# Optimization experiments

Measured on AMD Instinct MI355X. Metric: run time of the kernel, lower is better.

Reference implementation:

```python
import jax, jax.numpy as jnp
import numpy as np

B, S, DIM, H, HD = 2, 2048, 512, 8, 64
VD = DIM // H  # 64
QK = H * HD


def setup_inputs() -> dict:
    key = jax.random.key(0)
    k1, k2, k3, k4, k5 = jax.random.split(key, 5)
    x = jax.random.normal(k1, (B, S, DIM), dtype=jnp.float32)
    mask = jax.random.bernoulli(k2, 0.5, (B, S))
    # per-position rotation matrices, scaled to keep activations O(1)
    rotator = jax.random.normal(k3, (B, S, HD, HD), dtype=jnp.float32) / np.sqrt(HD)
    # torch Linear weights: [out_features, in_features], no bias
    W_trans = jax.random.normal(k4, (2 * QK + DIM, DIM), dtype=jnp.float32) / np.sqrt(DIM)
    W_o = jax.random.normal(k5, (DIM, DIM), dtype=jnp.float32) / np.sqrt(DIM)
    return {"x": x, "mask": mask, "rotator": rotator, "W_trans": W_trans, "W_o": W_o}


def _taylor_attention(qs, ks, vs, mask):
    # 2nd-order Taylor approximation of exp for softmax weights
    # qs/ks: [B,S,H,HD], vs: [B,S,H,VD], mask: [B,S] key mask
    scores = jnp.einsum('bqhd,bkhd->bhqk', qs, ks) / np.sqrt(HD)
    w = 1.0 + scores + 0.5 * scores * scores
    w = jnp.where(mask[:, None, None, :], w, 0.0)
    w = w / jnp.sum(w, axis=-1, keepdims=True)
    out = jnp.einsum('bhqk,bkhd->bqhd', w, vs)
    return out.reshape(out.shape[0], out.shape[1], -1)  # [B,S,DIM]


def reference(x, mask, rotator, W_trans, W_o):
    t = x @ W_trans.T  # [B,S,2*QK+DIM]
    qs = t[..., :QK].reshape(B, S, H, HD)
    ks = t[..., QK:2 * QK].reshape(B, S, H, HD)
    vs = t[..., 2 * QK:].reshape(B, S, H, VD)
    sel = mask[..., None, None]
    qs = jnp.where(sel, jnp.einsum('bsij,bshj->bshi', rotator, qs), qs)
    ks = jnp.where(sel, jnp.einsum('bsij,bshj->bshi', rotator, ks), ks)
    out = _taylor_attention(qs, ks, vs, mask)
    return out @ W_o.T
```

## Files before the change

kernel.cpp:

```cpp
#include <hip/hip_runtime.h>
#include <hip/hip_bf16.h>

#define B_    2
#define S_    2048
#define DIM_  512
#define H_    8
#define HD_   64
#define TOUT_ 1536
#define ROWS_ (B_ * S_)

typedef unsigned short ushort_t;
typedef __attribute__((ext_vector_type(8))) __bf16 bf16x8;
typedef __attribute__((ext_vector_type(4))) float floatx4;

#define AS_GLB __attribute__((address_space(1)))
#define AS_LDS __attribute__((address_space(3)))

__device__ __forceinline__ unsigned short f2bfu(float f) {
    unsigned u = __float_as_uint(f);
    unsigned r = (u + 0x7fffu + ((u >> 16) & 1u)) >> 16;
    return (unsigned short)r;
}
__device__ __forceinline__ bf16x8 cvt8(const float* p) {
    float4 a = *reinterpret_cast<const float4*>(p);
    float4 b = *reinterpret_cast<const float4*>(p + 4);
    ushort_t o[8] = {f2bfu(a.x), f2bfu(a.y), f2bfu(a.z), f2bfu(a.w),
                     f2bfu(b.x), f2bfu(b.y), f2bfu(b.z), f2bfu(b.w)};
    return *reinterpret_cast<bf16x8*>(o);
}

__global__ void tmha_mask(const unsigned char* mb, int* wm) {
    __shared__ int s_bf, s_f, s_u8;
    int tid = threadIdx.x;
    if (tid == 0) { s_bf = 0; s_f = 0; s_u8 = 0; }
    __syncthreads();
    int cbf = 0, cf = 0, cu8 = 0;
    for (int i = tid; i < 4096; i += 256) {
        unsigned char v = mb[i];
        if (v == 0x3F || v == 0x80) {
            cf++;
            if ((i & 3) == 1) cbf++;
        } else if (v != 0 && (i & 3) != 0) {
            cu8++;
        }
    }
    atomicAdd(&s_bf, cbf); atomicAdd(&s_f, cf); atomicAdd(&s_u8, cu8);
    __syncthreads();
    int cls = (s_bf > 0) ? 2 : (s_f > 0) ? 3 : (s_u8 > 0) ? 0 : 1;
    for (int i = tid; i < ROWS_; i += 256) {
        int v;
        if (cls == 0)      v = (mb[i] != 0);
        else if (cls == 1) v = (reinterpret_cast<const int*>(mb)[i] != 0);
        else if (cls == 2) v = ((reinterpret_cast<const unsigned short*>(mb)[i] & 0x7fffu) != 0);
        else               v = ((reinterpret_cast<const unsigned int*>(mb)[i] & 0x7fffffffu) != 0);
        wm[i] = v;
    }
}

#define XN4_  (ROWS_ * DIM_ / 4)
#define WTN4_ (TOUT_ * DIM_ / 4)
#define WON4_ (DIM_ * DIM_ / 4)
__global__ __launch_bounds__(256) void cast3_bf16(const float* __restrict__ x,
                                                  const float* __restrict__ wt,
                                                  const float* __restrict__ wo,
                                                  ushort_t* __restrict__ xb,
                                                  ushort_t* __restrict__ wtb,
                                                  ushort_t* __restrict__ wob) {
    int i = blockIdx.x * 256 + threadIdx.x;
    const float* s; ushort_t* d; int off;
    if (i < XN4_)              { s = x;  d = xb;  off = i; }
    else if (i < XN4_ + WTN4_) { s = wt; d = wtb; off = i - XN4_; }
    else                       { s = wo; d = wob; off = i - XN4_ - WTN4_; }
    float4 v = reinterpret_cast<const float4*>(s)[off];
    ushort_t o[4] = {f2bfu(v.x), f2bfu(v.y), f2bfu(v.z), f2bfu(v.w)};
    reinterpret_cast<uint2*>(d)[off] = *reinterpret_cast<uint2*>(o);
}

template <int TM, int N, int K, bool OUT_BF16>
__global__ __launch_bounds__(256) void mfma_gemm_bt(const ushort_t* __restrict__ A,
                                                    const ushort_t* __restrict__ Bm,
                                                    void* __restrict__ Cout) {
    constexpr int FM = (TM + 31) / 32;
    __shared__ __align__(16) ushort_t As[TM * 64];
    __shared__ __align__(16) ushort_t Bs[128 * 64];
    int tid = threadIdx.x;
    int lane = tid & 63;
    int wv = tid >> 6;
    int wm = wv >> 1, wn = wv & 1;
    int quad = lane >> 4;
    int mrow = lane & 15;
    int bx = blockIdx.x;
    int by = blockIdx.y;

    floatx4 acc[FM][4];
#pragma unroll
    for (int i = 0; i < FM; i++)
#pragma unroll
        for (int j = 0; j < 4; j++) acc[i][j] = (floatx4){0.f, 0.f, 0.f, 0.f};

    for (int k0 = 0; k0 < K; k0 += 64) {
#pragma unroll
        for (int t = 0; t < TM / 32; t++) {
            int p = (wv * (TM / 32) + t) * 64 + lane;
            int row = p >> 3, cp = p & 7;
            int gc = cp ^ (row & 7);
            const ushort_t* ga = A + (size_t)(by * TM + row) * K + k0 + gc * 8;
            __builtin_amdgcn_global_load_lds((const AS_GLB unsigned int*)ga,
                                             (AS_LDS unsigned int*)&As[(size_t)(wv * (TM / 32) + t) * 64 * 8],
                                             16, 0, 0);
        }
#pragma unroll
        for (int t = 0; t < 4; t++) {
            int p = (wv * 4 + t) * 64 + lane;
            int row = p >> 3, cp = p & 7;
            int gc = cp ^ (row & 7);
            const ushort_t* gb = Bm + (size_t)(bx * 128 + row) * K + k0 + gc * 8;
            __builtin_amdgcn_global_load_lds((const AS_GLB unsigned int*)gb,
                                             (AS_LDS unsigned int*)&Bs[(size_t)(wv * 4 + t) * 64 * 8],
                                             16, 0, 0);
        }
        __syncthreads();
#pragma unroll
        for (int ks = 0; ks < 64; ks += 32) {
            int c = (ks >> 3) + quad;
            bf16x8 af[FM], bf[4];
#pragma unroll
            for (int i = 0; i < FM; i++) {
                int row = wm * (TM / 2) + i * 16 + mrow;
                int pos = row * 8 + (c ^ (row & 7));
                af[i] = *reinterpret_cast<const bf16x8*>(&As[pos * 8]);
            }
#pragma unroll
            for (int j = 0; j < 4; j++) {
                int row = wn * 64 + j * 16 + mrow;
                int pos = row * 8 + (c ^ (row & 7));
                bf[j] = *reinterpret_cast<const bf16x8*>(&Bs[pos * 8]);
            }
#pragma unroll
            for (int i = 0; i < FM; i++)
#pragma unroll
                for (int j = 0; j < 4; j++)
                    acc[i][j] = __builtin_amdgcn_mfma_f32_16x16x32_bf16(af[i], bf[j], acc[i][j], 0, 0, 0);
        }
        __syncthreads();
    }

    int col0 = bx * 128 + wn * 64 + mrow;
    int row0 = by * TM + wm * (TM / 2) + quad * 4;
    if constexpr (OUT_BF16) {
        ushort_t* C = reinterpret_cast<ushort_t*>(Cout);
#pragma unroll
        for (int i = 0; i < FM; i++)
#pragma unroll
            for (int j = 0; j < 4; j++)
#pragma unroll
                for (int r = 0; r < 4; r++)
                    C[(size_t)(row0 + i * 16 + r) * N + col0 + j * 16] = f2bfu(acc[i][j][r]);
    } else {
        float* C = reinterpret_cast<float*>(Cout);
#pragma unroll
        for (int i = 0; i < FM; i++)
#pragma unroll
            for (int j = 0; j < 4; j++)
#pragma unroll
                for (int r = 0; r < 4; r++)
                    C[(size_t)(row0 + i * 16 + r) * N + col0 + j * 16] = acc[i][j][r];
    }
}

__global__ __launch_bounds__(256) void rot_qk_mfma(const ushort_t* __restrict__ t,
                                                   const float* __restrict__ rotG,
                                                   const int* __restrict__ wm,
                                                   ushort_t* __restrict__ Qb,
                                                   ushort_t* __restrict__ Kb) {
    int lane = threadIdx.x & 63;
    int wv = threadIdx.x >> 6;
    int row = blockIdx.x * 4 + wv;
    int b = row >> 11, s = row & 2047;
    int lm = lane & 15, quad = lane >> 4;
    const ushort_t* trow = t + (size_t)row * TOUT_;
    int kb = s >> 4, l = s & 15;

    if (wm[row]) {
        bf16x8 af[2];
#pragma unroll
        for (int kc = 0; kc < 2; kc++)
            af[kc] = *reinterpret_cast<const bf16x8*>(trow + lm * 64 + kc * 32 + quad * 8);

        const float* R = rotG + (size_t)row * 4096;
        floatx4 dacc[4];
#pragma unroll
        for (int nb = 0; nb < 4; nb++) dacc[nb] = (floatx4){0.f, 0.f, 0.f, 0.f};
#pragma unroll
        for (int nb = 0; nb < 4; nb++)
#pragma unroll
            for (int kc = 0; kc < 2; kc++) {
                bf16x8 bfr = cvt8(R + (size_t)(nb * 16 + lm) * 64 + kc * 32 + quad * 8);
                dacc[nb] = __builtin_amdgcn_mfma_f32_16x16x32_bf16(af[kc], bfr, dacc[nb], 0, 0, 0);
            }
#pragma unroll
        for (int nb = 0; nb < 4; nb++)
#pragma unroll
            for (int r = 0; r < 4; r++) {
                int vec = quad * 4 + r;
                int hh = vec & 7;
                ushort_t v = f2bfu(dacc[nb][r]);
                if (vec >= 8) {
                    int c = nb * 2 + (lm >> 3), e = lm & 7;
                    Kb[(((size_t)(b * 8 + hh) * 128 + kb) * 8 + c) * 128 + l * 8 + e] = v;
                } else {
                    Qb[((size_t)(b * 8 + hh) * 2048 + s) * 64 + nb * 16 + lm] = v;
                }
            }
    } else {
#pragma unroll
        for (int nb = 0; nb < 4; nb++)
#pragma unroll
            for (int r = 0; r < 4; r++) {
                int vec = quad * 4 + r;
                int hh = vec & 7;
                ushort_t v = trow[vec * 64 + nb * 16 + lm];
                if (vec >= 8) {
                    int c = nb * 2 + (lm >> 3), e = lm & 7;
                    Kb[(((size_t)(b * 8 + hh) * 128 + kb) * 8 + c) * 128 + l * 8 + e] = v;
                } else {
                    Qb[((size_t)(b * 8 + hh) * 2048 + s) * 64 + nb * 16 + lm] = v;
                }
            }
    }
}

__global__ __launch_bounds__(256) void prep_vt(const ushort_t* __restrict__ t,
                                               const int* __restrict__ wm,
                                               ushort_t* __restrict__ VtG) {
    __shared__ ushort_t tile[64][72];
    __shared__ float mrow[64];
    int st = blockIdx.x;
    int bh = blockIdx.y;
    int b = bh >> 3, h = bh & 7;
    int tid = threadIdx.x;
    if (tid < 64) mrow[tid] = wm[b * 2048 + st * 64 + tid] ? 1.0f : 0.0f;
#pragma unroll
    for (int i = 0; i < 2; i++) {
        int q = i * 256 + tid;
        int r = q >> 3, c8 = (q & 7) * 8;
        uint4 v = *reinterpret_cast<const uint4*>(
            t + (size_t)(b * 2048 + st * 64 + r) * TOUT_ + 1024 + h * 64 + c8);
        *reinterpret_cast<uint4*>(&tile[r][c8]) = v;
    }
    __syncthreads();
#pragma unroll
    for (int i = 0; i < 8; i++) {
        int e = i * 256 + tid;
        int d = e >> 5, sl = (e & 31) * 2;
        unsigned u0 = (mrow[sl]     != 0.f) ? (unsigned)tile[sl][d]     : 0u;
        unsigned u1 = (mrow[sl + 1] != 0.f) ? (unsigned)tile[sl + 1][d] : 0u;
        *reinterpret_cast<unsigned int*>(VtG + ((size_t)bh * 65 + d) * 2048 + st * 64 + sl) = u0 | (u1 << 16);
    }
    if (tid < 32) {
        int sl = tid * 2;
        unsigned m0 = mrow[sl]     != 0.f ? 0x3F80u : 0u;
        unsigned m1 = mrow[sl + 1] != 0.f ? 0x3F80u : 0u;
        *reinterpret_cast<unsigned int*>(VtG + ((size_t)bh * 65 + 64) * 2048 + st * 64 + sl) = m0 | (m1 << 16);
    }
}

__global__ __launch_bounds__(256) void tmha_attn_mfma(const ushort_t* __restrict__ Qb,
                                                      const ushort_t* __restrict__ KbF,
                                                      const ushort_t* __restrict__ VtG,
                                                      float* __restrict__ numer,
                                                      float* __restrict__ den) {
    __shared__ __align__(16) ushort_t Vs[2][520 * 8];
    __shared__ __align__(16) ushort_t Ps[512 * 8];
    int tid = threadIdx.x;
    int lane = tid & 63;
    int wv = tid >> 6;
    int lm = lane & 15;
    int quad = lane >> 4;
    int qt = blockIdx.x;
    int h = blockIdx.y;
    int z = blockIdx.z;
    int b = z >> 1;
    int ks = z & 1;
    int bh = b * 8 + h;

    const ushort_t* Kf  = KbF + (size_t)bh * 128 * 1024;
    const ushort_t* Vbh = VtG + (size_t)bh * 65 * 2048;

    bf16x8 qf[2];
    {
        const ushort_t* qp = Qb + ((size_t)bh * 2048 + qt * 64 + wv * 16 + lm) * 64 + quad * 8;
        qf[0] = *reinterpret_cast<const bf16x8*>(qp);
        qf[1] = *reinterpret_cast<const bf16x8*>(qp + 32);
    }

    bf16x8 vzero;
    *reinterpret_cast<uint4*>(&vzero) = (uint4){0u, 0u, 0u, 0u};

    floatx4 oacc[5];
#pragma unroll
    for (int j = 0; j < 5; j++) oacc[j] = (floatx4){0.f, 0.f, 0.f, 0.f};

    bf16x8 kr[4][2];
    auto loadK = [&](int kt) {
        int kb = kt >> 4;
#pragma unroll
        for (int j = 0; j < 4; j++)
#pragma unroll
            for (int kc = 0; kc < 2; kc++)
                kr[j][kc] = *reinterpret_cast<const bf16x8*>(
                    Kf + (((size_t)(kb + j) * 8 + kc * 4 + quad) * 16 + lm) * 8);
    };
    auto stageV = [&](int buf, int kt) {
#pragma unroll
        for (int t4 = 0; t4 < 2; t4++) {
            int p = (wv * 2 + t4) * 64 + lane;
            int row = p >> 3, cp = p & 7;
            int gc = cp ^ (row & 7);
            const ushort_t* g = Vbh + (size_t)row * 2048 + kt + gc * 8;
            __builtin_amdgcn_global_load_lds((const AS_GLB unsigned int*)g,
                                             (AS_LDS unsigned int*)&Vs[buf][(wv * 2 + t4) * 64 * 8],
                                             16, 0, 0);
        }
        if (tid < 8) {
            const ushort_t* g = Vbh + (size_t)64 * 2048 + kt + tid * 8;
            __builtin_amdgcn_global_load_lds((const AS_GLB unsigned int*)g,
                                             (AS_LDS unsigned int*)&Vs[buf][512 * 8],
                                             16, 0, 0);
        }
    };

    int kt0 = ks * 1024;
    stageV(0, kt0);
    loadK(kt0);
    int buf = 0;
#pragma unroll 1
    for (int tt = 0; tt < 16; tt++) {
        int ktn = (tt == 15) ? kt0 : kt0 + (tt + 1) * 64;
        __syncthreads();
        stageV(buf ^ 1, ktn);

        floatx4 sacc[4];
#pragma unroll
        for (int j = 0; j < 4; j++) sacc[j] = (floatx4){0.f, 0.f, 0.f, 0.f};
#pragma unroll
        for (int j = 0; j < 4; j++)
#pragma unroll
            for (int kc = 0; kc < 2; kc++)
                sacc[j] = __builtin_amdgcn_mfma_f32_16x16x32_bf16(qf[kc], kr[j][kc], sacc[j], 0, 0, 0);

        loadK(ktn);

#pragma unroll
        for (int j = 0; j < 4; j++)
#pragma unroll
            for (int r = 0; r < 4; r++) {
                float s = sacc[j][r];
                float wgt = fmaf(s, fmaf(s, 0.0078125f, 0.125f), 1.0f);
                int m = wv * 16 + quad * 4 + r;
                int col = j * 16 + lm;
                int cw = col >> 3;
                int pos = m * 8 + (cw ^ (m & 7));
                Ps[pos * 8 + (col & 7)] = f2bfu(wgt);
            }
        asm volatile("s_waitcnt lgkmcnt(0)" ::: "memory");
        __builtin_amdgcn_sched_barrier(0);

        int qrow_l = wv * 16 + lm;
        bf16x8 pa[2];
#pragma unroll
        for (int kc = 0; kc < 2; kc++) {
            int c = kc * 4 + quad;
            int ppos = qrow_l * 8 + (c ^ (qrow_l & 7));
            pa[kc] = *reinterpret_cast<const bf16x8*>(&Ps[ppos * 8]);
        }
#pragma unroll
        for (int j = 0; j < 5; j++) {
            int vrow = (j < 4) ? (j * 16 + lm) : 64;
#pragma unroll
            for (int kc = 0; kc < 2; kc++) {
                int c = kc * 4 + quad;
                int vpos = vrow * 8 + (c ^ (vrow & 7));
                bf16x8 vb = *reinterpret_cast<const bf16x8*>(&Vs[buf][vpos * 8]);
                if (j == 4 && lm != 0) vb = vzero;
                oacc[j] = __builtin_amdgcn_mfma_f32_16x16x32_bf16(pa[kc], vb, oacc[j], 0, 0, 0);
            }
        }
        buf ^= 1;
    }

#pragma unroll
    for (int j = 0; j < 4; j++)
#pragma unroll
        for (int r = 0; r < 4; r++) {
            int qrow = b * 2048 + qt * 64 + wv * 16 + quad * 4 + r;
            numer[((size_t)ks * ROWS_ + qrow) * DIM_ + h * 64 + j * 16 + lm] = oacc[j][r];
        }
    if (lm == 0) {
#pragma unroll
        for (int r = 0; r < 4; r++) {
            int qrow = b * 2048 + qt * 64 + wv * 16 + quad * 4 + r;
            den[((size_t)ks * ROWS_ + qrow) * 8 + h] = oacc[4][r];
        }
    }
}

__global__ __launch_bounds__(256) void attn_combine(const float* __restrict__ numer,
                                                    const float* __restrict__ den,
                                                    ushort_t* __restrict__ attnAb) {
    int i = blockIdx.x * 256 + threadIdx.x;
    int row = i >> 7;
    int c4 = (i & 127) * 4;
    int h = c4 >> 6;
    float4 n0 = *reinterpret_cast<const float4*>(&numer[(size_t)row * DIM_ + c4]);
    float4 n1 = *reinterpret_cast<const float4*>(&numer[((size_t)ROWS_ + row) * DIM_ + c4]);
    float d = den[(size_t)row * 8 + h] + den[((size_t)ROWS_ + row) * 8 + h];
    float inv = 1.0f / d;
    ushort_t o[4] = {f2bfu((n0.x + n1.x) * inv), f2bfu((n0.y + n1.y) * inv),
                     f2bfu((n0.z + n1.z) * inv), f2bfu((n0.w + n1.w) * inv)};
    *reinterpret_cast<uint2*>(&attnAb[(size_t)row * DIM_ + c4]) = *reinterpret_cast<uint2*>(o);
}

extern "C" void kernel_launch(void* const* d_in, const int* in_sizes, int n_in,
                              void* d_out, int out_size, void* d_ws, size_t ws_size,
                              hipStream_t stream) {
    (void)in_sizes; (void)n_in; (void)out_size; (void)ws_size;
    const float* x    = (const float*)d_in[0];
    const void*  mask = d_in[1];
    const float* rot  = (const float*)d_in[2];
    const float* Wt   = (const float*)d_in[3];
    const float* Wo   = (const float*)d_in[4];

    char* ws = (char*)d_ws;
    int* wmask       = (int*)(ws + 64);
    ushort_t* t      = (ushort_t*)(ws + 32768);
    ushort_t* Xb     = (ushort_t*)(ws + 25198592);
    ushort_t* Wtb    = (ushort_t*)(ws + 29392896);
    ushort_t* Wob    = (ushort_t*)(ws + 30965760);
    ushort_t* Qb     = (ushort_t*)(ws + 31490048);
    ushort_t* Kb     = (ushort_t*)(ws + 35684352);
    ushort_t* VtG    = (ushort_t*)(ws + 39878656);
    ushort_t* attnAb = (ushort_t*)(ws + 44138496);
    float* numer     = (float*)(ws + 32768);
    float* den       = (float*)(ws + 32768 + 16777216);

    tmha_mask<<<1, 256, 0, stream>>>((const unsigned char*)mask, wmask);

    cast3_bf16<<<(XN4_ + WTN4_ + WON4_) / 256, 256, 0, stream>>>(x, Wt, Wo, Xb, Wtb, Wob);

    {
        dim3 grid(TOUT_ / 128, ROWS_ / 64);
        mfma_gemm_bt<64, TOUT_, DIM_, true><<<grid, 256, 0, stream>>>(Xb, Wtb, (void*)t);
    }

    rot_qk_mfma<<<ROWS_ / 4, 256, 0, stream>>>(t, rot, wmask, Qb, Kb);

    {
        dim3 grid(32, 16);
        prep_vt<<<grid, 256, 0, stream>>>(t, wmask, VtG);
    }

    {
        dim3 grid(32, 8, 4);
        tmha_attn_mfma<<<grid, 256, 0, stream>>>(Qb, Kb, VtG, numer, den);
    }
    attn_combine<<<(ROWS_ * 128) / 256, 256, 0, stream>>>(numer, den, attnAb);

    {
        dim3 grid(DIM_ / 128, ROWS_ / 32);
        mfma_gemm_bt<32, DIM_, DIM_, false><<<grid, 256, 0, stream>>>(attnAb, Wob, d_out);
    }
}
```

Before: 194.0 us.

## Fuse mask into cast kernel, fold combine into output GEMM, retune attention pipeline

The mask-decoding kernel is folded into the input cast kernel as an extra block, so one launch is saved. The split-K combine (summing the two partial numerators and denominators, then normalizing) moves into the A-tile load of the output GEMM, which removes a kernel and the bf16 round trip of the intermediate. The attention loop becomes a manually unrolled ping-pong with separate V buffers. It reads the mask row straight from global memory instead of LDS, adds setprio around the MFMAs and uses an explicit vmcnt wait plus barrier. The cost is that the output GEMM now does the fp32 reads and the reduction redundantly for each of its 4 column blocks.

```diff
diff --git a/kernel.cpp b/kernel.cpp
--- a/kernel.cpp
+++ b/kernel.cpp
@@ -29,43 +29,46 @@
     return *reinterpret_cast<bf16x8*>(o);
 }
 
-__global__ void tmha_mask(const unsigned char* mb, int* wm) {
-    __shared__ int s_bf, s_f, s_u8;
-    int tid = threadIdx.x;
-    if (tid == 0) { s_bf = 0; s_f = 0; s_u8 = 0; }
-    __syncthreads();
-    int cbf = 0, cf = 0, cu8 = 0;
-    for (int i = tid; i < 4096; i += 256) {
-        unsigned char v = mb[i];
-        if (v == 0x3F || v == 0x80) {
-            cf++;
-            if ((i & 3) == 1) cbf++;
-        } else if (v != 0 && (i & 3) != 0) {
-            cu8++;
-        }
-    }
-    atomicAdd(&s_bf, cbf); atomicAdd(&s_f, cf); atomicAdd(&s_u8, cu8);
-    __syncthreads();
-    int cls = (s_bf > 0) ? 2 : (s_f > 0) ? 3 : (s_u8 > 0) ? 0 : 1;
-    for (int i = tid; i < ROWS_; i += 256) {
-        int v;
-        if (cls == 0)      v = (mb[i] != 0);
-        else if (cls == 1) v = (reinterpret_cast<const int*>(mb)[i] != 0);
-        else if (cls == 2) v = ((reinterpret_cast<const unsigned short*>(mb)[i] & 0x7fffu) != 0);
-        else               v = ((reinterpret_cast<const unsigned int*>(mb)[i] & 0x7fffffffu) != 0);
-        wm[i] = v;
-    }
-}
-
 #define XN4_  (ROWS_ * DIM_ / 4)
 #define WTN4_ (TOUT_ * DIM_ / 4)
 #define WON4_ (DIM_ * DIM_ / 4)
-__global__ __launch_bounds__(256) void cast3_bf16(const float* __restrict__ x,
-                                                  const float* __restrict__ wt,
-                                                  const float* __restrict__ wo,
-                                                  ushort_t* __restrict__ xb,
-                                                  ushort_t* __restrict__ wtb,
-                                                  ushort_t* __restrict__ wob) {
+#define CASTBLKS_ ((XN4_ + WTN4_ + WON4_) / 256)
+__global__ __launch_bounds__(256) void prep_inputs(const float* __restrict__ x,
+                                                   const float* __restrict__ wt,
+                                                   const float* __restrict__ wo,
+                                                   const unsigned char* __restrict__ mb,
+                                                   ushort_t* __restrict__ xb,
+                                                   ushort_t* __restrict__ wtb,
+                                                   ushort_t* __restrict__ wob,
+                                                   int* __restrict__ wm) {
+    if (blockIdx.x >= CASTBLKS_) {
+        __shared__ int s_bf, s_f, s_u8;
+        int tid = threadIdx.x;
+        if (tid == 0) { s_bf = 0; s_f = 0; s_u8 = 0; }
+        __syncthreads();
+        int cbf = 0, cf = 0, cu8 = 0;
+        for (int i = tid; i < 4096; i += 256) {
+            unsigned char v = mb[i];
+            if (v == 0x3F || v == 0x80) {
+                cf++;
+                if ((i & 3) == 1) cbf++;
+            } else if (v != 0 && (i & 3) != 0) {
+                cu8++;
+            }
+        }
+        atomicAdd(&s_bf, cbf); atomicAdd(&s_f, cf); atomicAdd(&s_u8, cu8);
+        __syncthreads();
+        int cls = (s_bf > 0) ? 2 : (s_f > 0) ? 3 : (s_u8 > 0) ? 0 : 1;
+        for (int i = tid; i < ROWS_; i += 256) {
+            int v;
+            if (cls == 0)      v = (mb[i] != 0);
+            else if (cls == 1) v = (reinterpret_cast<const int*>(mb)[i] != 0);
+            else if (cls == 2) v = ((reinterpret_cast<const unsigned short*>(mb)[i] & 0x7fffu) != 0);
+            else               v = ((reinterpret_cast<const unsigned int*>(mb)[i] & 0x7fffffffu) != 0);
+            wm[i] = v;
+        }
+        return;
+    }
     int i = blockIdx.x * 256 + threadIdx.x;
     const float* s; ushort_t* d; int off;
     if (i < XN4_)              { s = x;  d = xb;  off = i; }
@@ -168,6 +171,90 @@
     }
 }
 
+__global__ __launch_bounds__(256) void gemm2_fused(const float* __restrict__ numer,
+                                                   const float* __restrict__ den,
+                                                   const ushort_t* __restrict__ Bm,
+                                                   float* __restrict__ C) {
+    constexpr int TM = 32, N = DIM_, K = DIM_;
+    __shared__ __align__(16) ushort_t As[TM * 64];
+    __shared__ __align__(16) ushort_t Bs[128 * 64];
+    int tid = threadIdx.x;
+    int lane = tid & 63;
+    int wv = tid >> 6;
+    int wm = wv >> 1, wn = wv & 1;
+    int quad = lane >> 4;
+    int mrow = lane & 15;
+    int bx = blockIdx.x;
+    int by = blockIdx.y;
+
+    floatx4 acc[4];
+#pragma unroll
+    for (int j = 0; j < 4; j++) acc[j] = (floatx4){0.f, 0.f, 0.f, 0.f};
+
+    for (int k0 = 0; k0 < K; k0 += 64) {
+        {
+            int p = tid;
+            int row = p >> 3, cp = p & 7;
+            int arow = by * TM + row;
+            int col0 = k0 + cp * 8;
+            int hh = col0 >> 6;
+            float dsum = den[(size_t)arow * 8 + hh] + den[((size_t)ROWS_ + arow) * 8 + hh];
+            float inv = 1.0f / dsum;
+            const float* n0 = &numer[(size_t)arow * DIM_ + col0];
+            const float* n1 = &numer[((size_t)ROWS_ + arow) * DIM_ + col0];
+            float4 a0 = *reinterpret_cast<const float4*>(n0);
+            float4 a1 = *reinterpret_cast<const float4*>(n0 + 4);
+            float4 b0 = *reinterpret_cast<const float4*>(n1);
+            float4 b1 = *reinterpret_cast<const float4*>(n1 + 4);
+            ushort_t o[8] = {f2bfu((a0.x + b0.x) * inv), f2bfu((a0.y + b0.y) * inv),
+                             f2bfu((a0.z + b0.z) * inv), f2bfu((a0.w + b0.w) * inv),
+                             f2bfu((a1.x + b1.x) * inv), f2bfu((a1.y + b1.y) * inv),
+                             f2bfu((a1.z + b1.z) * inv), f2bfu((a1.w + b1.w) * inv)};
+            int pos = row * 8 + (cp ^ (row & 7));
+            *reinterpret_cast<uint4*>(&As[pos * 8]) = *reinterpret_cast<const uint4*>(o);
+        }
+#pragma unroll
+        for (int t = 0; t < 4; t++) {
+            int p = (wv * 4 + t) * 64 + lane;
+            int row = p >> 3, cp = p & 7;
+            int gc = cp ^ (row & 7);
+            const ushort_t* gb = Bm + (size_t)(bx * 128 + row) * K + k0 + gc * 8;
+            __builtin_amdgcn_global_load_lds((const AS_GLB unsigned int*)gb,
+                                             (AS_LDS unsigned int*)&Bs[(size_t)(wv * 4 + t) * 64 * 8],
+                                             16, 0, 0);
+        }
+        __syncthreads();
+#pragma unroll
+        for (int ks = 0; ks < 64; ks += 32) {
+            int c = (ks >> 3) + quad;
+            bf16x8 af, bf[4];
+            {
+                int row = wm * 16 + mrow;
+                int pos = row * 8 + (c ^ (row & 7));
+                af = *reinterpret_cast<const bf16x8*>(&As[pos * 8]);
+            }
+#pragma unroll
+            for (int j = 0; j < 4; j++) {
+                int row = wn * 64 + j * 16 + mrow;
+                int pos = row * 8 + (c ^ (row & 7));
+                bf[j] = *reinterpret_cast<const bf16x8*>(&Bs[pos * 8]);
+            }
+#pragma unroll
+            for (int j = 0; j < 4; j++)
+                acc[j] = __builtin_amdgcn_mfma_f32_16x16x32_bf16(af, bf[j], acc[j], 0, 0, 0);
+        }
+        __syncthreads();
+    }
+
+    int col0 = bx * 128 + wn * 64 + mrow;
+    int row0 = by * TM + wm * 16 + quad * 4;
+#pragma unroll
+    for (int j = 0; j < 4; j++)
+#pragma unroll
+        for (int r = 0; r < 4; r++)
+            C[(size_t)(row0 + r) * N + col0 + j * 16] = acc[j][r];
+}
+
 __global__ __launch_bounds__(256) void rot_qk_mfma(const ushort_t* __restrict__ t,
                                                    const float* __restrict__ rotG,
                                                    const int* __restrict__ wm,
@@ -270,7 +357,8 @@
                                                       const ushort_t* __restrict__ VtG,
                                                       float* __restrict__ numer,
                                                       float* __restrict__ den) {
-    __shared__ __align__(16) ushort_t Vs[2][520 * 8];
+    __shared__ __align__(16) ushort_t VsA[512 * 8];
+    __shared__ __align__(16) ushort_t VsB[512 * 8];
     __shared__ __align__(16) ushort_t Ps[512 * 8];
     int tid = threadIdx.x;
     int lane = tid & 63;
@@ -284,8 +372,9 @@
     int ks = z & 1;
     int bh = b * 8 + h;
 
-    const ushort_t* Kf  = KbF + (size_t)bh * 128 * 1024;
-    const ushort_t* Vbh = VtG + (size_t)bh * 65 * 2048;
+    const ushort_t* Kf   = KbF + (size_t)bh * 128 * 1024;
+    const ushort_t* Vbh  = VtG + (size_t)bh * 65 * 2048;
+    const ushort_t* Mrow = Vbh + (size_t)64 * 2048;
 
     bf16x8 qf[2];
     {
@@ -311,7 +400,7 @@
                 kr[j][kc] = *reinterpret_cast<const bf16x8*>(
                     Kf + (((size_t)(kb + j) * 8 + kc * 4 + quad) * 16 + lm) * 8);
     };
-    auto stageV = [&](int buf, int kt) {
+    auto stageV = [&](ushort_t* Vw, int kt) {
 #pragma unroll
         for (int t4 = 0; t4 < 2; t4++) {
             int p = (wv * 2 + t4) * 64 + lane;
@@ -319,35 +408,30 @@
             int gc = cp ^ (row & 7);
             const ushort_t* g = Vbh + (size_t)row * 2048 + kt + gc * 8;
             __builtin_amdgcn_global_load_lds((const AS_GLB unsigned int*)g,
-                                             (AS_LDS unsigned int*)&Vs[buf][(wv * 2 + t4) * 64 * 8],
+                                             (AS_LDS unsigned int*)&Vw[(wv * 2 + t4) * 64 * 8],
                                              16, 0, 0);
         }
-        if (tid < 8) {
-            const ushort_t* g = Vbh + (size_t)64 * 2048 + kt + tid * 8;
-            __builtin_amdgcn_global_load_lds((const AS_GLB unsigned int*)g,
-                                             (AS_LDS unsigned int*)&Vs[buf][512 * 8],
-                                             16, 0, 0);
-        }
     };
 
-    int kt0 = ks * 1024;
-    stageV(0, kt0);
-    loadK(kt0);
-    int buf = 0;
-#pragma unroll 1
-    for (int tt = 0; tt < 16; tt++) {
-        int ktn = (tt == 15) ? kt0 : kt0 + (tt + 1) * 64;
-        __syncthreads();
-        stageV(buf ^ 1, ktn);
+    auto tile = [&](const ushort_t* Vr, ushort_t* Vw, int kt, int ktn) {
+        bf16x8 mvb[2];
+#pragma unroll
+        for (int kc = 0; kc < 2; kc++)
+            mvb[kc] = *reinterpret_cast<const bf16x8*>(Mrow + kt + (kc * 4 + quad) * 8);
+        __builtin_amdgcn_sched_barrier(0);
+        stageV(Vw, ktn);
+        __builtin_amdgcn_sched_barrier(0);
 
         floatx4 sacc[4];
 #pragma unroll
         for (int j = 0; j < 4; j++) sacc[j] = (floatx4){0.f, 0.f, 0.f, 0.f};
+        __builtin_amdgcn_s_setprio(1);
 #pragma unroll
         for (int j = 0; j < 4; j++)
 #pragma unroll
             for (int kc = 0; kc < 2; kc++)
                 sacc[j] = __builtin_amdgcn_mfma_f32_16x16x32_bf16(qf[kc], kr[j][kc], sacc[j], 0, 0, 0);
+        __builtin_amdgcn_s_setprio(0);
 
         loadK(ktn);
 
@@ -374,19 +458,41 @@
             int ppos = qrow_l * 8 + (c ^ (qrow_l & 7));
             pa[kc] = *reinterpret_cast<const bf16x8*>(&Ps[ppos * 8]);
         }
-#pragma unroll
-        for (int j = 0; j < 5; j++) {
-            int vrow = (j < 4) ? (j * 16 + lm) : 64;
+        __builtin_amdgcn_s_setprio(1);
+#pragma unroll
+        for (int j = 0; j < 4; j++) {
+            int vrow = j * 16 + lm;
 #pragma unroll
             for (int kc = 0; kc < 2; kc++) {
                 int c = kc * 4 + quad;
                 int vpos = vrow * 8 + (c ^ (vrow & 7));
-                bf16x8 vb = *reinterpret_cast<const bf16x8*>(&Vs[buf][vpos * 8]);
-                if (j == 4 && lm != 0) vb = vzero;
+                bf16x8 vb = *reinterpret_cast<const bf16x8*>(&Vr[vpos * 8]);
                 oacc[j] = __builtin_amdgcn_mfma_f32_16x16x32_bf16(pa[kc], vb, oacc[j], 0, 0, 0);
             }
         }
-        buf ^= 1;
+#pragma unroll
+        for (int kc = 0; kc < 2; kc++) {
+            bf16x8 vb = (lm == 0) ? mvb[kc] : vzero;
+            oacc[4] = __builtin_amdgcn_mfma_f32_16x16x32_bf16(pa[kc], vb, oacc[4], 0, 0, 0);
+        }
+        __builtin_amdgcn_s_setprio(0);
+
+        __builtin_amdgcn_sched_barrier(0);
+        asm volatile("s_waitcnt vmcnt(8)" ::: "memory");
+        __builtin_amdgcn_s_barrier();
+    };
+
+    int kt0 = ks * 1024;
+    stageV(VsA, kt0);
+    loadK(kt0);
+    __syncthreads();
+#pragma unroll 1
+    for (int tt = 0; tt < 8; tt++) {
+        int kt = kt0 + tt * 128;
+        int kt1 = kt + 64;
+        int kt2 = (tt == 7) ? kt0 : kt + 128;
+        tile(VsA, VsB, kt, kt1);
+        tile(VsB, VsA, kt1, kt2);
     }
 
 #pragma unroll
@@ -403,22 +509,6 @@
             den[((size_t)ks * ROWS_ + qrow) * 8 + h] = oacc[4][r];
         }
     }
-}
-
-__global__ __launch_bounds__(256) void attn_combine(const float* __restrict__ numer,
-                                                    const float* __restrict__ den,
-                                                    ushort_t* __restrict__ attnAb) {
-    int i = blockIdx.x * 256 + threadIdx.x;
-    int row = i >> 7;
-    int c4 = (i & 127) * 4;
-    int h = c4 >> 6;
-    float4 n0 = *reinterpret_cast<const float4*>(&numer[(size_t)row * DIM_ + c4]);
-    float4 n1 = *reinterpret_cast<const float4*>(&numer[((size_t)ROWS_ + row) * DIM_ + c4]);
-    float d = den[(size_t)row * 8 + h] + den[((size_t)ROWS_ + row) * 8 + h];
-    float inv = 1.0f / d;
-    ushort_t o[4] = {f2bfu((n0.x + n1.x) * inv), f2bfu((n0.y + n1.y) * inv),
-                     f2bfu((n0.z + n1.z) * inv), f2bfu((n0.w + n1.w) * inv)};
-    *reinterpret_cast<uint2*>(&attnAb[(size_t)row * DIM_ + c4]) = *reinterpret_cast<uint2*>(o);
 }
 
 extern "C" void kernel_launch(void* const* d_in, const int* in_sizes, int n_in,
@@ -440,13 +530,11 @@
     ushort_t* Qb     = (ushort_t*)(ws + 31490048);
     ushort_t* Kb     = (ushort_t*)(ws + 35684352);
     ushort_t* VtG    = (ushort_t*)(ws + 39878656);
-    ushort_t* attnAb = (ushort_t*)(ws + 44138496);
     float* numer     = (float*)(ws + 32768);
     float* den       = (float*)(ws + 32768 + 16777216);
 
-    tmha_mask<<<1, 256, 0, stream>>>((const unsigned char*)mask, wmask);
-
-    cast3_bf16<<<(XN4_ + WTN4_ + WON4_) / 256, 256, 0, stream>>>(x, Wt, Wo, Xb, Wtb, Wob);
+    prep_inputs<<<CASTBLKS_ + 1, 256, 0, stream>>>(x, Wt, Wo, (const unsigned char*)mask,
+                                                   Xb, Wtb, Wob, wmask);
 
     {
         dim3 grid(TOUT_ / 128, ROWS_ / 64);
@@ -464,10 +552,9 @@
         dim3 grid(32, 8, 4);
         tmha_attn_mfma<<<grid, 256, 0, stream>>>(Qb, Kb, VtG, numer, den);
     }
-    attn_combine<<<(ROWS_ * 128) / 256, 256, 0, stream>>>(numer, den, attnAb);
 
     {
         dim3 grid(DIM_ / 128, ROWS_ / 32);
-        mfma_gemm_bt<32, DIM_, DIM_, false><<<grid, 256, 0, stream>>>(attnAb, Wob, d_out);
-    }
-}
+        gemm2_fused<<<grid, 256, 0, stream>>>(numer, den, Wob, (float*)d_out);
+    }
+}
```

After: 201.2 us. +3.7%, slower.
